# Performance work log

Hardware: AMD Instinct MI355X
Metric: run time of the kernel (lower is better)

The kernel has to match this reference:

```python
import jax, jax.numpy as jnp
import numpy as np

D_MODEL = 1024
LAYER_IDX = 5
D_FF = 4096
SPARSITY = 0.9
TOKENS = 8192
IN_UP = D_MODEL * (LAYER_IDX + 1)  # 6144


def _sparse_weight(rng, out_f, in_f, sparsity):
    """Row-wise k-sparse weight matrix mimicking SparseLinear's padded-CSR:
    each output row keeps k = round(in_f*(1-sparsity)) live columns,
    values ~ U(-b, b) with b = 1/sqrt(effective_fan_in)."""
    k = max(1, round(in_f * (1.0 - sparsity)))
    bound = 1.0 / np.sqrt(max(1.0, in_f * (1.0 - sparsity)))
    scores = rng.random((out_f, in_f))
    # top-k per row -> boolean mask
    thresh = np.partition(scores, in_f - k, axis=1)[:, in_f - k][:, None]
    mask = scores >= thresh
    W = (rng.uniform(-bound, bound, (out_f, in_f)).astype(np.float32)) * mask
    return jnp.asarray(W), jnp.asarray(mask)


def setup_inputs() -> dict:
    key = jax.random.key(0)
    x = jax.random.normal(key, (TOKENS, IN_UP), dtype=jnp.float32)
    rng = np.random.default_rng(0)
    W_up, mask_up = _sparse_weight(rng, D_FF, IN_UP, SPARSITY)
    W_down, mask_down = _sparse_weight(rng, D_MODEL, D_FF, SPARSITY)
    return {"ffn_input_cat": x, "W_up": W_up, "W_down": W_down,
            "mask_up": mask_up, "mask_down": mask_down}


def reference(ffn_input_cat, W_up, W_down, mask_up, mask_down):
    # fc_down(gelu(fc_up(x))); SparseLinear == masked dense linear, no bias.
    # torch F.gelu default is the exact (erf) gelu.
    h = jax.nn.gelu(ffn_input_cat @ (W_up * mask_up).T, approximate=False)  # [T, d_ff]
    return h @ (W_down * mask_down).T  # [T, d_model]
```

## Files before the change

### kernel.cpp

```cpp
#include <hip/hip_runtime.h>
#include <cstdint>
#include <cstddef>

typedef unsigned short u16;
typedef __attribute__((ext_vector_type(8))) short  bf16x8;
typedef __attribute__((ext_vector_type(4))) float  f32x4;

__device__ __forceinline__ u16 f2bf(float f) {
    unsigned u = __float_as_uint(f);
    unsigned r = (u + 0x7FFFu + ((u >> 16) & 1u)) >> 16;
    return (u16)r;
}

__device__ __forceinline__ void async_lds16(const u16* g, u16* l) {
    __builtin_amdgcn_global_load_lds(
        (const __attribute__((address_space(1))) unsigned int*)g,
        (__attribute__((address_space(3))) unsigned int*)l,
        16, 0, 0);
}

__global__ __launch_bounds__(256) void cvt_bf16_kernel(const float* __restrict__ src,
                                                       u16* __restrict__ dst, int n8) {
    int i = blockIdx.x * 256 + threadIdx.x;
    if (i >= n8) return;
    const float4* s = (const float4*)src;
    float4 a = s[2 * i];
    float4 b = s[2 * i + 1];
    union { bf16x8 v; u16 e[8]; } o;
    o.e[0] = f2bf(a.x); o.e[1] = f2bf(a.y); o.e[2] = f2bf(a.z); o.e[3] = f2bf(a.w);
    o.e[4] = f2bf(b.x); o.e[5] = f2bf(b.y); o.e[6] = f2bf(b.z); o.e[7] = f2bf(b.w);
    ((bf16x8*)dst)[i] = o.v;
}

#define BM 128
#define BN 128
#define BK 32

template<bool GELU, typename OutT>
__global__ __launch_bounds__(256) void gemm_bt(const u16* __restrict__ A,
                                               const u16* __restrict__ B,
                                               OutT* __restrict__ C,
                                               int M, int N, int K) {
    __shared__ __align__(16) u16 As[BM * BK];
    __shared__ __align__(16) u16 Bs[BN * BK];

    const int tid  = threadIdx.x;
    const int wave = tid >> 6;
    const int lane = tid & 63;
    const int quad = lane >> 4;
    const int r16  = lane & 15;

    const int m0 = blockIdx.x * BM;
    const int n0 = blockIdx.y * BN;

    const int wm = (wave >> 1) * 64;
    const int wn = (wave & 1) * 64;

    const int srow = tid >> 2;
    const int scol = (tid & 3) * 8;

    f32x4 acc[4][4] = {};

    const u16* gA0 = A + (size_t)(m0 + srow) * K + scol;
    const u16* gA1 = A + (size_t)(m0 + 64 + srow) * K + scol;
    const u16* gB0 = B + (size_t)(n0 + srow) * K + scol;
    const u16* gB1 = B + (size_t)(n0 + 64 + srow) * K + scol;

    u16* lA0 = &As[wave * 512];
    u16* lA1 = &As[2048 + wave * 512];
    u16* lB0 = &Bs[wave * 512];
    u16* lB1 = &Bs[2048 + wave * 512];

    for (int k0 = 0; k0 < K; k0 += BK) {
        async_lds16(gA0 + k0, lA0);
        async_lds16(gA1 + k0, lA1);
        async_lds16(gB0 + k0, lB0);
        async_lds16(gB1 + k0, lB1);
        __syncthreads();

        bf16x8 af[4], bf[4];
#pragma unroll
        for (int i = 0; i < 4; i++) {
            af[i] = *(const bf16x8*)&As[(wm + i * 16 + r16) * BK + quad * 8];
            bf[i] = *(const bf16x8*)&Bs[(wn + i * 16 + r16) * BK + quad * 8];
        }
#pragma unroll
        for (int mi = 0; mi < 4; mi++)
#pragma unroll
            for (int ni = 0; ni < 4; ni++)
                acc[mi][ni] = __builtin_amdgcn_mfma_f32_16x16x32_bf16(
                    af[mi], bf[ni], acc[mi][ni], 0, 0, 0);
        __syncthreads();
    }

#pragma unroll
    for (int mi = 0; mi < 4; mi++) {
#pragma unroll
        for (int r = 0; r < 4; r++) {
            size_t rowoff = (size_t)(m0 + wm + mi * 16 + quad * 4 + r) * N;
#pragma unroll
            for (int ni = 0; ni < 4; ni++) {
                int col = n0 + wn + ni * 16 + r16;
                float v = acc[mi][ni][r];
                if constexpr (GELU)
                    v = 0.5f * v * (1.0f + erff(v * 0.70710678118654752f));
                if constexpr (sizeof(OutT) == 2)
                    ((u16*)C)[rowoff + col] = f2bf(v);
                else
                    ((float*)C)[rowoff + col] = v;
            }
        }
    }
}

extern "C" void kernel_launch(void* const* d_in, const int* in_sizes, int n_in,
                              void* d_out, int out_size, void* d_ws, size_t ws_size,
                              hipStream_t stream) {
    const int T   = 8192;
    const int DIN = 6144;
    const int DFF = 4096;
    const int DM  = 1024;

    const float* x  = (const float*)d_in[0];
    const float* wu = (const float*)d_in[1];
    const float* wd = (const float*)d_in[2];
    float* out = (float*)d_out;

    u16* xb  = (u16*)d_ws;
    u16* wub = xb  + (size_t)T * DIN;
    u16* wdb = wub + (size_t)DFF * DIN;
    u16* hb  = wdb + (size_t)DM * DFF;

    {
        int n8 = T * DIN / 8;
        cvt_bf16_kernel<<<n8 / 256, 256, 0, stream>>>(x, xb, n8);
    }
    {
        int n8 = DFF * DIN / 8;
        cvt_bf16_kernel<<<n8 / 256, 256, 0, stream>>>(wu, wub, n8);
    }
    {
        int n8 = DM * DFF / 8;
        cvt_bf16_kernel<<<n8 / 256, 256, 0, stream>>>(wd, wdb, n8);
    }

    dim3 g1(T / BM, DFF / BN);
    gemm_bt<true, u16><<<g1, 256, 0, stream>>>(xb, wub, hb, T, DFF, DIN);

    dim3 g2(T / BM, DM / BN);
    gemm_bt<false, float><<<g2, 256, 0, stream>>>(hb, wdb, out, T, DM, DFF);
}
```

Measured before the change: 1.054 ms.

## Split-K the down projection and reorder GEMM grid to iterate N fastest

Both GEMMs now launch with the N tile index on blockIdx.x, so neighbouring blocks share the same A row panel and can reuse it in L2. The down-projection GEMM is split four ways along K into fp32 partial buffers placed in workspace that is no longer needed. A separate float4 kernel then sums the four partials into the output. This raises the block count for the small second GEMM, at the cost of extra global traffic for writing and re-reading the partials plus one more launch.

New measurement: 1.105 ms. 1.05x slower.

```diff
diff --git a/kernel.cpp b/kernel.cpp
--- a/kernel.cpp
+++ b/kernel.cpp
@@ -36,11 +36,12 @@
 #define BN 128
 #define BK 32
 
-template<bool GELU, typename OutT>
+template<bool GELU, bool NFAST, typename OutT>
 __global__ __launch_bounds__(256) void gemm_bt(const u16* __restrict__ A,
                                                const u16* __restrict__ B,
                                                OutT* __restrict__ C,
-                                               int M, int N, int K) {
+                                               int M, int N, int K,
+                                               int lda, int ldb, int ldc) {
     __shared__ __align__(16) u16 As[BM * BK];
     __shared__ __align__(16) u16 Bs[BN * BK];
 
@@ -50,8 +51,13 @@
     const int quad = lane >> 4;
     const int r16  = lane & 15;
 
-    const int m0 = blockIdx.x * BM;
-    const int n0 = blockIdx.y * BN;
+    const int m0 = (NFAST ? blockIdx.y : blockIdx.x) * BM;
+    const int n0 = (NFAST ? blockIdx.x : blockIdx.y) * BN;
+
+    const size_t kbase = (size_t)blockIdx.z * K;
+    A += kbase;
+    B += kbase;
+    C += (size_t)blockIdx.z * M * ldc;
 
     const int wm = (wave >> 1) * 64;
     const int wn = (wave & 1) * 64;
@@ -61,10 +67,10 @@
 
     f32x4 acc[4][4] = {};
 
-    const u16* gA0 = A + (size_t)(m0 + srow) * K + scol;
-    const u16* gA1 = A + (size_t)(m0 + 64 + srow) * K + scol;
-    const u16* gB0 = B + (size_t)(n0 + srow) * K + scol;
-    const u16* gB1 = B + (size_t)(n0 + 64 + srow) * K + scol;
+    const u16* gA0 = A + (size_t)(m0 + srow) * lda + scol;
+    const u16* gA1 = A + (size_t)(m0 + 64 + srow) * lda + scol;
+    const u16* gB0 = B + (size_t)(n0 + srow) * ldb + scol;
+    const u16* gB1 = B + (size_t)(n0 + 64 + srow) * ldb + scol;
 
     u16* lA0 = &As[wave * 512];
     u16* lA1 = &As[2048 + wave * 512];
@@ -97,7 +103,7 @@
     for (int mi = 0; mi < 4; mi++) {
 #pragma unroll
         for (int r = 0; r < 4; r++) {
-            size_t rowoff = (size_t)(m0 + wm + mi * 16 + quad * 4 + r) * N;
+            size_t rowoff = (size_t)(m0 + wm + mi * 16 + quad * 4 + r) * ldc;
 #pragma unroll
             for (int ni = 0; ni < 4; ni++) {
                 int col = n0 + wn + ni * 16 + r16;
@@ -113,6 +119,23 @@
     }
 }
 
+__global__ __launch_bounds__(256) void reduce4_kernel(const float4* __restrict__ p,
+                                                      float4* __restrict__ out,
+                                                      int n4, int stride4) {
+    int i = blockIdx.x * 256 + threadIdx.x;
+    if (i >= n4) return;
+    float4 a = p[i];
+    float4 b = p[i + stride4];
+    float4 c = p[i + 2 * stride4];
+    float4 d = p[i + 3 * stride4];
+    float4 o;
+    o.x = (a.x + b.x) + (c.x + d.x);
+    o.y = (a.y + b.y) + (c.y + d.y);
+    o.z = (a.z + b.z) + (c.z + d.z);
+    o.w = (a.w + b.w) + (c.w + d.w);
+    out[i] = o;
+}
+
 extern "C" void kernel_launch(void* const* d_in, const int* in_sizes, int n_in,
                               void* d_out, int out_size, void* d_ws, size_t ws_size,
                               hipStream_t stream) {
@@ -120,33 +143,31 @@
     const int DIN = 6144;
     const int DFF = 4096;
     const int DM  = 1024;
+    const int KS  = 4;
 
     const float* x  = (const float*)d_in[0];
     const float* wu = (const float*)d_in[1];
     const float* wd = (const float*)d_in[2];
-    float* out = (float*)d_out;
 
     u16* xb  = (u16*)d_ws;
     u16* wub = xb  + (size_t)T * DIN;
     u16* wdb = wub + (size_t)DFF * DIN;
     u16* hb  = wdb + (size_t)DM * DFF;
+    float* part = (float*)d_ws;
 
-    {
-        int n8 = T * DIN / 8;
-        cvt_bf16_kernel<<<n8 / 256, 256, 0, stream>>>(x, xb, n8);
-    }
-    {
-        int n8 = DFF * DIN / 8;
-        cvt_bf16_kernel<<<n8 / 256, 256, 0, stream>>>(wu, wub, n8);
-    }
-    {
-        int n8 = DM * DFF / 8;
-        cvt_bf16_kernel<<<n8 / 256, 256, 0, stream>>>(wd, wdb, n8);
-    }
+    cvt_bf16_kernel<<<T * DIN / 8 / 256, 256, 0, stream>>>(x, xb, T * DIN / 8);
+    cvt_bf16_kernel<<<DFF * DIN / 8 / 256, 256, 0, stream>>>(wu, wub, DFF * DIN / 8);
+    cvt_bf16_kernel<<<DM * DFF / 8 / 256, 256, 0, stream>>>(wd, wdb, DM * DFF / 8);
 
-    dim3 g1(T / BM, DFF / BN);
-    gemm_bt<true, u16><<<g1, 256, 0, stream>>>(xb, wub, hb, T, DFF, DIN);
+    dim3 g1(DFF / BN, T / BM, 1);
+    gemm_bt<true, true, u16><<<g1, 256, 0, stream>>>(xb, wub, hb,
+                                                     T, DFF, DIN, DIN, DIN, DFF);
 
-    dim3 g2(T / BM, DM / BN);
-    gemm_bt<false, float><<<g2, 256, 0, stream>>>(hb, wdb, out, T, DM, DFF);
+    dim3 g2(DM / BN, T / BM, KS);
+    gemm_bt<false, true, float><<<g2, 256, 0, stream>>>(hb, wdb, part,
+                                                        T, DM, DFF / KS, DFF, DFF, DM);
+
+    int n4 = T * DM / 4;
+    reduce4_kernel<<<n4 / 256, 256, 0, stream>>>((const float4*)part, (float4*)d_out,
+                                                 n4, n4);
 }
```

## Double BK, XOR-swizzle LDS layout, swap grid order, fuse conversion kernels

Applied to the files above, without the earlier changes.

Raises the GEMM K-tile from 32 to 64 so each barrier pair covers twice as many MFMAs. It also XOR-swizzles the LDS column placement to avoid bank conflicts on fragment reads, and swaps the grid axes so neighbouring blocks share the same A rows for L2 reuse. The three fp32-to-bf16 conversion launches are merged into one kernel. LDS use doubles per block, which may lower occupancy.

New measurement: 937.7 us. 11.1% less time.

```diff
diff --git a/kernel.cpp b/kernel.cpp
--- a/kernel.cpp
+++ b/kernel.cpp
@@ -19,28 +19,33 @@
         16, 0, 0);
 }
 
-__global__ __launch_bounds__(256) void cvt_bf16_kernel(const float* __restrict__ src,
-                                                       u16* __restrict__ dst, int n8) {
+__global__ __launch_bounds__(256) void cvt3_kernel(const float* __restrict__ s0, u16* __restrict__ d0, int n0,
+                                                   const float* __restrict__ s1, u16* __restrict__ d1, int n1,
+                                                   const float* __restrict__ s2, u16* __restrict__ d2, int n2) {
     int i = blockIdx.x * 256 + threadIdx.x;
-    if (i >= n8) return;
-    const float4* s = (const float4*)src;
-    float4 a = s[2 * i];
-    float4 b = s[2 * i + 1];
+    const float* s; u16* d;
+    if (i < n0)            { s = s0; d = d0; }
+    else if (i < n0 + n1)  { s = s1; d = d1; i -= n0; }
+    else                   { s = s2; d = d2; i -= n0 + n1; if (i >= n2) return; }
+    const float4* sp = (const float4*)s;
+    float4 a = sp[2 * i];
+    float4 b = sp[2 * i + 1];
     union { bf16x8 v; u16 e[8]; } o;
     o.e[0] = f2bf(a.x); o.e[1] = f2bf(a.y); o.e[2] = f2bf(a.z); o.e[3] = f2bf(a.w);
     o.e[4] = f2bf(b.x); o.e[5] = f2bf(b.y); o.e[6] = f2bf(b.z); o.e[7] = f2bf(b.w);
-    ((bf16x8*)dst)[i] = o.v;
+    ((bf16x8*)d)[i] = o.v;
 }
 
 #define BM 128
 #define BN 128
-#define BK 32
+#define BK 64
 
 template<bool GELU, typename OutT>
 __global__ __launch_bounds__(256) void gemm_bt(const u16* __restrict__ A,
                                                const u16* __restrict__ B,
                                                OutT* __restrict__ C,
-                                               int M, int N, int K) {
+                                               int M, int N, int K,
+                                               int lda, int ldb, int ldc) {
     __shared__ __align__(16) u16 As[BM * BK];
     __shared__ __align__(16) u16 Bs[BN * BK];
 
@@ -50,46 +55,54 @@
     const int quad = lane >> 4;
     const int r16  = lane & 15;
 
-    const int m0 = blockIdx.x * BM;
-    const int n0 = blockIdx.y * BN;
+    const int n0 = blockIdx.x * BN;
+    const int m0 = blockIdx.y * BM;
 
     const int wm = (wave >> 1) * 64;
     const int wn = (wave & 1) * 64;
 
-    const int srow = tid >> 2;
-    const int scol = (tid & 3) * 8;
+    const int srow = tid >> 3;
+    const int g8   = (tid & 7) ^ (srow & 7);
+    const int scol = g8 * 8;
+
+    const u16* gA[4]; const u16* gB[4];
+    u16* lA[4]; u16* lB[4];
+#pragma unroll
+    for (int i = 0; i < 4; i++) {
+        gA[i] = A + (size_t)(m0 + 32 * i + srow) * lda + scol;
+        gB[i] = B + (size_t)(n0 + 32 * i + srow) * ldb + scol;
+        lA[i] = &As[(32 * i + 8 * wave) * BK];
+        lB[i] = &Bs[(32 * i + 8 * wave) * BK];
+    }
 
     f32x4 acc[4][4] = {};
 
-    const u16* gA0 = A + (size_t)(m0 + srow) * K + scol;
-    const u16* gA1 = A + (size_t)(m0 + 64 + srow) * K + scol;
-    const u16* gB0 = B + (size_t)(n0 + srow) * K + scol;
-    const u16* gB1 = B + (size_t)(n0 + 64 + srow) * K + scol;
-
-    u16* lA0 = &As[wave * 512];
-    u16* lA1 = &As[2048 + wave * 512];
-    u16* lB0 = &Bs[wave * 512];
-    u16* lB1 = &Bs[2048 + wave * 512];
-
     for (int k0 = 0; k0 < K; k0 += BK) {
-        async_lds16(gA0 + k0, lA0);
-        async_lds16(gA1 + k0, lA1);
-        async_lds16(gB0 + k0, lB0);
-        async_lds16(gB1 + k0, lB1);
+#pragma unroll
+        for (int i = 0; i < 4; i++) async_lds16(gA[i] + k0, lA[i]);
+#pragma unroll
+        for (int i = 0; i < 4; i++) async_lds16(gB[i] + k0, lB[i]);
         __syncthreads();
 
-        bf16x8 af[4], bf[4];
 #pragma unroll
-        for (int i = 0; i < 4; i++) {
-            af[i] = *(const bf16x8*)&As[(wm + i * 16 + r16) * BK + quad * 8];
-            bf[i] = *(const bf16x8*)&Bs[(wn + i * 16 + r16) * BK + quad * 8];
+        for (int ks = 0; ks < 2; ks++) {
+            bf16x8 af[4], bf[4];
+#pragma unroll
+            for (int i = 0; i < 4; i++) {
+                int ra = wm + i * 16 + r16;
+                int rb = wn + i * 16 + r16;
+                int pa = ((ks * 4 + quad) ^ (ra & 7)) * 8;
+                int pb = ((ks * 4 + quad) ^ (rb & 7)) * 8;
+                af[i] = *(const bf16x8*)&As[ra * BK + pa];
+                bf[i] = *(const bf16x8*)&Bs[rb * BK + pb];
+            }
+#pragma unroll
+            for (int mi = 0; mi < 4; mi++)
+#pragma unroll
+                for (int ni = 0; ni < 4; ni++)
+                    acc[mi][ni] = __builtin_amdgcn_mfma_f32_16x16x32_bf16(
+                        af[mi], bf[ni], acc[mi][ni], 0, 0, 0);
         }
-#pragma unroll
-        for (int mi = 0; mi < 4; mi++)
-#pragma unroll
-            for (int ni = 0; ni < 4; ni++)
-                acc[mi][ni] = __builtin_amdgcn_mfma_f32_16x16x32_bf16(
-                    af[mi], bf[ni], acc[mi][ni], 0, 0, 0);
         __syncthreads();
     }
 
@@ -97,7 +110,7 @@
     for (int mi = 0; mi < 4; mi++) {
 #pragma unroll
         for (int r = 0; r < 4; r++) {
-            size_t rowoff = (size_t)(m0 + wm + mi * 16 + quad * 4 + r) * N;
+            size_t rowoff = (size_t)(m0 + wm + mi * 16 + quad * 4 + r) * ldc;
 #pragma unroll
             for (int ni = 0; ni < 4; ni++) {
                 int col = n0 + wn + ni * 16 + r16;
@@ -124,29 +137,23 @@
     const float* x  = (const float*)d_in[0];
     const float* wu = (const float*)d_in[1];
     const float* wd = (const float*)d_in[2];
-    float* out = (float*)d_out;
 
     u16* xb  = (u16*)d_ws;
     u16* wub = xb  + (size_t)T * DIN;
     u16* wdb = wub + (size_t)DFF * DIN;
     u16* hb  = wdb + (size_t)DM * DFF;
 
-    {
-        int n8 = T * DIN / 8;
-        cvt_bf16_kernel<<<n8 / 256, 256, 0, stream>>>(x, xb, n8);
-    }
-    {
-        int n8 = DFF * DIN / 8;
-        cvt_bf16_kernel<<<n8 / 256, 256, 0, stream>>>(wu, wub, n8);
-    }
-    {
-        int n8 = DM * DFF / 8;
-        cvt_bf16_kernel<<<n8 / 256, 256, 0, stream>>>(wd, wdb, n8);
-    }
+    const int n8x  = T * DIN / 8;
+    const int n8wu = DFF * DIN / 8;
+    const int n8wd = DM * DFF / 8;
+    cvt3_kernel<<<(n8x + n8wu + n8wd) / 256, 256, 0, stream>>>(
+        x, xb, n8x, wu, wub, n8wu, wd, wdb, n8wd);
 
-    dim3 g1(T / BM, DFF / BN);
-    gemm_bt<true, u16><<<g1, 256, 0, stream>>>(xb, wub, hb, T, DFF, DIN);
+    dim3 g1(DFF / BN, T / BM);
+    gemm_bt<true, u16><<<g1, 256, 0, stream>>>(xb, wub, hb,
+                                               T, DFF, DIN, DIN, DIN, DFF);
 
-    dim3 g2(T / BM, DM / BN);
-    gemm_bt<false, float><<<g2, 256, 0, stream>>>(hb, wdb, out, T, DM, DFF);
+    dim3 g2(DM / BN, T / BM);
+    gemm_bt<false, float><<<g2, 256, 0, stream>>>(hb, wdb, (float*)d_out,
+                                                  T, DM, DFF, DFF, DFF, DM);
 }
```
